# Kernel optimization log

Hardware: AMD Instinct MI355X
Metric: run time of the kernel (lower is better)

The kernel has to match this reference:

```python
import jax, jax.numpy as jnp
import numpy as np

HIDDEN = 1024
HEADS = 16
HEAD_DIM = HIDDEN // HEADS
POS_DIM = 128
B, S = 2, 2048
ROPE_BASE = 10000.0


def setup_inputs() -> dict:
    key = jax.random.key(0)
    ks = jax.random.split(key, 8)
    sd = 1.0 / np.sqrt(HIDDEN)
    return {
        "x":   jax.random.normal(ks[0], (B, S, HIDDEN), dtype=jnp.float32),
        "W_q": jax.random.normal(ks[1], (HIDDEN, HIDDEN), dtype=jnp.float32) * sd,
        "W_k": jax.random.normal(ks[2], (HIDDEN, HIDDEN), dtype=jnp.float32) * sd,
        "W_v": jax.random.normal(ks[3], (HIDDEN, HIDDEN), dtype=jnp.float32) * sd,
        "W_o": jax.random.normal(ks[4], (HIDDEN, HIDDEN), dtype=jnp.float32) * sd,
        "repo_W1": jax.random.normal(ks[5], (HIDDEN, POS_DIM), dtype=jnp.float32) * sd,
        "repo_b1": jnp.zeros((POS_DIM,), dtype=jnp.float32),
        "repo_W2": jax.random.normal(ks[6], (POS_DIM, 1), dtype=jnp.float32) * (1.0 / np.sqrt(POS_DIM)),
        "repo_b2": jnp.zeros((1,), dtype=jnp.float32),
    }


def _repo_positions(x, W1, b1, W2, b2):
    # 2-layer MLP -> scalar per token; softplus + cumsum gives monotone learned positions
    h = jax.nn.gelu(jnp.einsum("bsd,dp->bsp", x, W1) + b1)
    raw = (jnp.einsum("bsp,po->bso", h, W2) + b2)[..., 0]      # (B, S)
    return jnp.cumsum(jax.nn.softplus(raw), axis=1)             # (B, S)


def _apply_rope(q, k, positions):
    # q, k: (B, S, H, Dh); positions: (B, S) continuous
    half = HEAD_DIM // 2
    inv_freq = 1.0 / (ROPE_BASE ** (jnp.arange(0, HEAD_DIM, 2, dtype=jnp.float32) / HEAD_DIM))
    angles = positions[:, :, None] * inv_freq                   # (B, S, half)
    cos = jnp.cos(angles)[:, :, None, :]                        # (B, S, 1, half)
    sin = jnp.sin(angles)[:, :, None, :]

    def rot(t):
        t1, t2 = t[..., :half], t[..., half:]
        return jnp.concatenate([t1 * cos - t2 * sin, t1 * sin + t2 * cos], axis=-1)

    return rot(q), rot(k)


def reference(x, W_q, W_k, W_v, W_o, repo_W1, repo_b1, repo_W2, repo_b2):
    scale = 1.0 / np.sqrt(HEAD_DIM)
    q = jnp.einsum("bsd,de->bse", x, W_q).reshape(B, S, HEADS, HEAD_DIM)
    k = jnp.einsum("bsd,de->bse", x, W_k).reshape(B, S, HEADS, HEAD_DIM)
    v = jnp.einsum("bsd,de->bse", x, W_v).reshape(B, S, HEADS, HEAD_DIM)

    positions = _repo_positions(x, repo_W1, repo_b1, repo_W2, repo_b2)
    q, k = _apply_rope(q, k, positions)

    # explicit O(S^2) attention, matching the torch module
    scores = jnp.einsum("bqhd,bkhd->bhqk", q, k) * scale        # (B, H, S, S)
    attn = jax.nn.softmax(scores, axis=-1)
    out = jnp.einsum("bhqk,bkhd->bqhd", attn, v)                # (B, S, H, Dh)
    out = out.reshape(B, S, HIDDEN)
    return jnp.einsum("bsd,de->bse", out, W_o)
```

## Files before the change

### kernel.cpp

```cpp
#include <hip/hip_runtime.h>
#include <hip/hip_bf16.h>
#include <math.h>

#define HIDDEN 1024
#define HEADS 16
#define HEAD_DIM 64
#define POS_DIM 128
#define BATCH 2
#define SEQ 2048
#define TOKENS (BATCH * SEQ)

typedef _Float16 f16;
typedef __attribute__((ext_vector_type(8))) _Float16 f16x8;
typedef __attribute__((ext_vector_type(4))) _Float16 f16x4;
typedef __attribute__((ext_vector_type(4))) float f32x4;

__device__ __forceinline__ void glds16(const f16* g, f16* l) {
    __builtin_amdgcn_global_load_lds((const __attribute__((address_space(1))) unsigned int*)g,
                                     (__attribute__((address_space(3))) unsigned int*)l, 16, 0, 0);
}

__global__ __launch_bounds__(256) void cast_x_kernel(const float* __restrict__ x,
                                                     f16* __restrict__ o) {
    const int i = (blockIdx.x * 256 + threadIdx.x) * 8;
    const float4 u = *(const float4*)(x + i);
    const float4 v = *(const float4*)(x + i + 4);
    f16x8 r = {(f16)u.x, (f16)u.y, (f16)u.z, (f16)u.w,
               (f16)v.x, (f16)v.y, (f16)v.z, (f16)v.w};
    *(f16x8*)(o + i) = r;
}

__global__ __launch_bounds__(256) void cast_wt4_kernel(const float* __restrict__ W0,
                                                       const float* __restrict__ W1,
                                                       const float* __restrict__ W2,
                                                       const float* __restrict__ W3,
                                                       f16* __restrict__ Wt) {
    __shared__ float ts[32][33];
    const int t = threadIdx.x;
    const int z = blockIdx.z;
    const float* W = (z == 0) ? W0 : (z == 1) ? W1 : (z == 2) ? W2 : W3;
    f16* dst = Wt + (size_t)z * HIDDEN * HIDDEN;
    const int k0 = blockIdx.y * 32, n0 = blockIdx.x * 32;
    {
        const int r = t >> 3, c4 = (t & 7) * 4;
        const float4 u = *(const float4*)(W + (size_t)(k0 + r) * HIDDEN + n0 + c4);
        ts[r][c4 + 0] = u.x; ts[r][c4 + 1] = u.y; ts[r][c4 + 2] = u.z; ts[r][c4 + 3] = u.w;
    }
    __syncthreads();
    {
        const int r = t >> 3, c4 = (t & 7) * 4;
        f16* o = dst + (size_t)(n0 + r) * HIDDEN + k0 + c4;
        o[0] = (f16)ts[c4 + 0][r]; o[1] = (f16)ts[c4 + 1][r];
        o[2] = (f16)ts[c4 + 2][r]; o[3] = (f16)ts[c4 + 3][r];
    }
}

__global__ __launch_bounds__(256) void cast_w1t_kernel(const float* __restrict__ W1,
                                                       f16* __restrict__ Wh,
                                                       f16* __restrict__ Wl) {
    __shared__ float ts[32][33];
    const int t = threadIdx.x;
    const int k0 = blockIdx.y * 32, p0 = blockIdx.x * 32;
    {
        const int r = t >> 3, c4 = (t & 7) * 4;
        const float4 u = *(const float4*)(W1 + (size_t)(k0 + r) * POS_DIM + p0 + c4);
        ts[r][c4 + 0] = u.x; ts[r][c4 + 1] = u.y; ts[r][c4 + 2] = u.z; ts[r][c4 + 3] = u.w;
    }
    __syncthreads();
    {
        const int r = t >> 3, c4 = (t & 7) * 4;
        f16* oh = Wh + (size_t)(p0 + r) * HIDDEN + k0 + c4;
        f16* ol = Wl + (size_t)(p0 + r) * HIDDEN + k0 + c4;
#pragma unroll
        for (int u = 0; u < 4; ++u) {
            const float v = ts[c4 + u][r];
            const f16 hi = (f16)v;
            oh[u] = hi;
            ol[u] = (f16)(v - (float)hi);
        }
    }
}

__global__ __launch_bounds__(256, 3) void gemm_gll(const f16* __restrict__ A,
                                                   const f16* __restrict__ Bt,
                                                   f16* __restrict__ Cb,
                                                   float* __restrict__ Cf,
                                                   int N, int f16out) {
    __shared__ __align__(16) f16 As[128 * 64];
    __shared__ __align__(16) f16 Bs[128 * 64];
    const int tid = threadIdx.x;
    const int w = tid >> 6, lane = tid & 63;
    const int g = lane >> 4, c = lane & 15;
    const int m0 = blockIdx.y * 128, n0 = blockIdx.x * 128;
    const int wm = (w & 1) * 64, wn = (w >> 1) * 64;

    const int lrow = lane >> 3;
    const int lseg = (lane & 7) ^ lrow;
    const f16* gA = A + (size_t)(m0 + w * 32 + lrow) * 1024 + lseg * 8;
    const f16* gB = Bt + (size_t)(n0 + w * 32 + lrow) * 1024 + lseg * 8;
    f16* lA = &As[(w * 32) * 64];
    f16* lB = &Bs[(w * 32) * 64];

    f32x4 acc[4][4];
    const f32x4 z = {0.f, 0.f, 0.f, 0.f};
#pragma unroll
    for (int i = 0; i < 4; ++i)
#pragma unroll
        for (int j = 0; j < 4; ++j) acc[i][j] = z;

    const int rsw = c & 7;
    for (int k0 = 0; k0 < 1024; k0 += 64) {
        __syncthreads();
#pragma unroll
        for (int p = 0; p < 4; ++p) {
            glds16(gA + (size_t)p * 8 * 1024 + k0, lA + p * 8 * 64);
            glds16(gB + (size_t)p * 8 * 1024 + k0, lB + p * 8 * 64);
        }
        __syncthreads();
#pragma unroll
        for (int s = 0; s < 2; ++s) {
            f16x8 af[4], bf[4];
#pragma unroll
            for (int i = 0; i < 4; ++i)
                af[i] = *(const f16x8*)&As[(wm + i * 16 + c) * 64 + (((s * 4 + g) ^ rsw) * 8)];
#pragma unroll
            for (int j = 0; j < 4; ++j)
                bf[j] = *(const f16x8*)&Bs[(wn + j * 16 + c) * 64 + (((s * 4 + g) ^ rsw) * 8)];
#pragma unroll
            for (int i = 0; i < 4; ++i)
#pragma unroll
                for (int j = 0; j < 4; ++j)
                    acc[i][j] = __builtin_amdgcn_mfma_f32_16x16x32_f16(af[i], bf[j], acc[i][j], 0, 0, 0);
        }
    }
#pragma unroll
    for (int i = 0; i < 4; ++i)
#pragma unroll
        for (int j = 0; j < 4; ++j)
#pragma unroll
            for (int r = 0; r < 4; ++r) {
                const size_t off = (size_t)(m0 + wm + i * 16 + 4 * g + r) * N + n0 + wn + j * 16 + c;
                if (f16out) Cb[off] = (f16)acc[i][j][r];
                else Cf[off] = acc[i][j][r];
            }
}

__device__ __forceinline__ float gelu_tanh(float x) {
    const float kA = 0.7978845608028654f;
    return 0.5f * x * (1.0f + tanhf(kA * (x + 0.044715f * x * x * x)));
}

__global__ __launch_bounds__(256, 2) void repo_mfma(const float* __restrict__ x,
                                                    const f16* __restrict__ w1h,
                                                    const f16* __restrict__ w1l,
                                                    const float* __restrict__ b1,
                                                    const float* __restrict__ W2,
                                                    const float* __restrict__ b2,
                                                    float* __restrict__ raw) {
    __shared__ __align__(16) f16 Ash[64 * 32], Asl[64 * 32];
    __shared__ __align__(16) f16 Bsh[128 * 32], Bsl[128 * 32];
    __shared__ float red[4][64];
    const int tid = threadIdx.x;
    const int w = tid >> 6, lane = tid & 63;
    const int g = lane >> 4, c = lane & 15;
    const int m0 = blockIdx.x * 64;

    const int arow = tid >> 2, aseg = tid & 3;
    const int aslot = (aseg ^ ((arow ^ (arow >> 2)) & 3)) << 3;
    const float* gA = x + (size_t)(m0 + arow) * 1024 + aseg * 8;
    const f16* gBh0 = w1h + (size_t)arow * 1024 + aseg * 8;
    const f16* gBh1 = w1h + (size_t)(arow + 64) * 1024 + aseg * 8;
    const f16* gBl0 = w1l + (size_t)arow * 1024 + aseg * 8;
    const f16* gBl1 = w1l + (size_t)(arow + 64) * 1024 + aseg * 8;
    f16* sAh = &Ash[arow * 32 + aslot];
    f16* sAl = &Asl[arow * 32 + aslot];
    f16* sBh0 = &Bsh[arow * 32 + aslot];
    f16* sBh1 = &Bsh[(arow + 64) * 32 + aslot];
    f16* sBl0 = &Bsl[arow * 32 + aslot];
    f16* sBl1 = &Bsl[(arow + 64) * 32 + aslot];

    const int foff = ((g ^ ((c ^ (c >> 2)) & 3)) << 3);

    f32x4 acc[4][2];
    const f32x4 z = {0.f, 0.f, 0.f, 0.f};
#pragma unroll
    for (int i = 0; i < 4; ++i) { acc[i][0] = z; acc[i][1] = z; }

    float4 pa0 = *(const float4*)gA;
    float4 pa1 = *(const float4*)(gA + 4);
    f16x8 pbh0 = *(const f16x8*)gBh0, pbh1 = *(const f16x8*)gBh1;
    f16x8 pbl0 = *(const f16x8*)gBl0, pbl1 = *(const f16x8*)gBl1;

    for (int k0 = 0; k0 < 1024; k0 += 32) {
        __syncthreads();
        {
            const float av[8] = {pa0.x, pa0.y, pa0.z, pa0.w, pa1.x, pa1.y, pa1.z, pa1.w};
            f16x8 ah, al;
#pragma unroll
            for (int u = 0; u < 8; ++u) {
                const f16 hi = (f16)av[u];
                ah[u] = hi;
                al[u] = (f16)(av[u] - (float)hi);
            }
            *(f16x8*)sAh = ah; *(f16x8*)sAl = al;
            *(f16x8*)sBh0 = pbh0; *(f16x8*)sBh1 = pbh1;
            *(f16x8*)sBl0 = pbl0; *(f16x8*)sBl1 = pbl1;
        }
        __syncthreads();
        if (k0 + 32 < 1024) {
            pa0 = *(const float4*)(gA + k0 + 32);
            pa1 = *(const float4*)(gA + k0 + 36);
            pbh0 = *(const f16x8*)(gBh0 + k0 + 32);
            pbh1 = *(const f16x8*)(gBh1 + k0 + 32);
            pbl0 = *(const f16x8*)(gBl0 + k0 + 32);
            pbl1 = *(const f16x8*)(gBl1 + k0 + 32);
        }
        f16x8 ah[4], al[4], bh[2], bl[2];
#pragma unroll
        for (int i = 0; i < 4; ++i) {
            ah[i] = *(const f16x8*)&Ash[(i * 16 + c) * 32 + foff];
            al[i] = *(const f16x8*)&Asl[(i * 16 + c) * 32 + foff];
        }
#pragma unroll
        for (int j = 0; j < 2; ++j) {
            bh[j] = *(const f16x8*)&Bsh[(w * 32 + j * 16 + c) * 32 + foff];
            bl[j] = *(const f16x8*)&Bsl[(w * 32 + j * 16 + c) * 32 + foff];
        }
#pragma unroll
        for (int i = 0; i < 4; ++i)
#pragma unroll
            for (int j = 0; j < 2; ++j) {
                acc[i][j] = __builtin_amdgcn_mfma_f32_16x16x32_f16(ah[i], bh[j], acc[i][j], 0, 0, 0);
                acc[i][j] = __builtin_amdgcn_mfma_f32_16x16x32_f16(ah[i], bl[j], acc[i][j], 0, 0, 0);
                acc[i][j] = __builtin_amdgcn_mfma_f32_16x16x32_f16(al[i], bh[j], acc[i][j], 0, 0, 0);
            }
    }
    float b1v[2], w2v[2];
#pragma unroll
    for (int j = 0; j < 2; ++j) {
        const int col = w * 32 + j * 16 + c;
        b1v[j] = b1[col];
        w2v[j] = W2[col];
    }
    float part[4][4];
#pragma unroll
    for (int i = 0; i < 4; ++i)
#pragma unroll
        for (int r = 0; r < 4; ++r) {
            float s = 0.f;
#pragma unroll
            for (int j = 0; j < 2; ++j)
                s += gelu_tanh(acc[i][j][r] + b1v[j]) * w2v[j];
            s += __shfl_xor(s, 1, 64);
            s += __shfl_xor(s, 2, 64);
            s += __shfl_xor(s, 4, 64);
            s += __shfl_xor(s, 8, 64);
            part[i][r] = s;
        }
    if (c == 0)
#pragma unroll
        for (int i = 0; i < 4; ++i)
#pragma unroll
            for (int r = 0; r < 4; ++r)
                red[w][i * 16 + 4 * g + r] = part[i][r];
    __syncthreads();
    if (tid < 64)
        raw[m0 + tid] = red[0][tid] + red[1][tid] + red[2][tid] + red[3][tid] + b2[0];
}

__device__ __forceinline__ double softplus_d(double x) {
    return (x > 0.0) ? x + log1p(exp(-x)) : log1p(exp(x));
}

__global__ __launch_bounds__(256) void repo_cumsum_kernel(const float* __restrict__ raw,
                                                          float* __restrict__ pos) {
    __shared__ double bufA[256];
    __shared__ double bufB[256];
    const int b = blockIdx.x;
    const int t = threadIdx.x;
    const float* r = raw + (size_t)b * SEQ;

    double loc[8];
    double sum = 0.0;
#pragma unroll
    for (int i = 0; i < 8; ++i) {
        sum += softplus_d((double)r[t * 8 + i]);
        loc[i] = sum;
    }
    bufA[t] = sum;
    __syncthreads();

    double* src = bufA;
    double* dst = bufB;
    for (int off = 1; off < 256; off <<= 1) {
        double v = src[t];
        if (t >= off) v += src[t - off];
        dst[t] = v;
        __syncthreads();
        double* tmp = src; src = dst; dst = tmp;
    }
    const double excl = src[t] - sum;
#pragma unroll
    for (int i = 0; i < 8; ++i)
        pos[(size_t)b * SEQ + t * 8 + i] = (float)(excl + loc[i]);
}

__global__ __launch_bounds__(256) void sctab_kernel(const float* __restrict__ pos,
                                                    float* __restrict__ costab,
                                                    float* __restrict__ sintab) {
    const int idx = blockIdx.x * 256 + threadIdx.x;
    const int tok = idx >> 5, i = idx & 31;
    const double ang = (double)pos[tok] * exp(-(double)i * 0.28782313662425574);
    double sa, ca;
    sincos(ang, &sa, &ca);
    costab[idx] = (float)ca;
    sintab[idx] = (float)sa;
}

__global__ __launch_bounds__(256) void packkv_kernel(f16* __restrict__ qkv,
                                                     const float* __restrict__ costab,
                                                     const float* __restrict__ sintab,
                                                     f16* __restrict__ kfo,
                                                     f16* __restrict__ vfo) {
    __shared__ __align__(16) f16 kds[64][72];
    __shared__ __align__(16) f16 vds[64][72];
    const int t = threadIdx.x;
    const int s0 = blockIdx.x * 64;
    const int h = blockIdx.y, b = blockIdx.z;
    const int key = t >> 2, part = t & 3;
    const int tok = b * SEQ + s0 + key;
    {
        float cs[8], sn[8];
        *(float4*)cs       = *(const float4*)(costab + tok * 32 + part * 8);
        *(float4*)(cs + 4) = *(const float4*)(costab + tok * 32 + part * 8 + 4);
        *(float4*)sn       = *(const float4*)(sintab + tok * 32 + part * 8);
        *(float4*)(sn + 4) = *(const float4*)(sintab + tok * 32 + part * 8 + 4);
        f16* qrow = qkv + (size_t)tok * 3072 + h * HEAD_DIM;
        {
            f16x8 lo = *(const f16x8*)(qrow + part * 8);
            f16x8 hi = *(const f16x8*)(qrow + part * 8 + 32);
#pragma unroll
            for (int u = 0; u < 8; ++u) {
                const float l = (float)lo[u], hh = (float)hi[u];
                lo[u] = (f16)(l * cs[u] - hh * sn[u]);
                hi[u] = (f16)(l * sn[u] + hh * cs[u]);
            }
            *(f16x8*)(qrow + part * 8) = lo;
            *(f16x8*)(qrow + part * 8 + 32) = hi;
        }
        const f16* krow = qrow + 1024;
        {
            f16x8 lo = *(const f16x8*)(krow + part * 8);
            f16x8 hi = *(const f16x8*)(krow + part * 8 + 32);
#pragma unroll
            for (int u = 0; u < 8; ++u) {
                const float l = (float)lo[u], hh = (float)hi[u];
                kds[key][part * 8 + u]      = (f16)(l * cs[u] - hh * sn[u]);
                kds[key][32 + part * 8 + u] = (f16)(l * sn[u] + hh * cs[u]);
            }
        }
        const f16* vrow = qrow + 2048;
        f16x8 v0 = *(const f16x8*)(vrow + part * 16);
        f16x8 v1 = *(const f16x8*)(vrow + part * 16 + 8);
#pragma unroll
        for (int u = 0; u < 8; ++u) {
            vds[part * 16 + u][key] = v0[u];
            vds[part * 16 + 8 + u][key] = v1[u];
        }
    }
    __syncthreads();
    const size_t cb = ((size_t)((b * HEADS + h) * 32) + blockIdx.x) * 4096;
#pragma unroll
    for (int p = 0; p < 2; ++p) {
        const int idx = p * 256 + t;
        const int frag = idx >> 6, lane = idx & 63;
        const int jn = frag >> 1, half = frag & 1, g = lane >> 4, c = lane & 15;
        *(f16x8*)(kfo + cb + frag * 512 + lane * 8) =
            *(const f16x8*)(&kds[jn * 16 + c][half * 32 + g * 8]);
    }
#pragma unroll
    for (int p = 0; p < 4; ++p) {
        const int idx = p * 256 + t;
        const int frag = idx >> 6, lane = idx & 63;
        const int jd = frag >> 2, jn = frag & 3, g = lane >> 4, c = lane & 15;
        *(f16x4*)(vfo + cb + frag * 256 + lane * 4) =
            *(const f16x4*)(&vds[jd * 16 + c][jn * 16 + 4 * g]);
    }
}

__global__ __launch_bounds__(256, 2) void attn_f16(const f16* __restrict__ qkv,
                                                   const f16* __restrict__ kfr,
                                                   const f16* __restrict__ vfr,
                                                   f16* __restrict__ aof0,
                                                   f16* __restrict__ aof1,
                                                   float* __restrict__ lsb) {
    __shared__ __align__(16) f16 kls[4096];
    __shared__ __align__(16) f16 vls[4096];
    __shared__ __align__(16) f16 ot[4][32][72];
    const int tid = threadIdx.x;
    const int w = tid >> 6, lane = tid & 63;
    const int g = lane >> 4, c = lane & 15;

    const int wid = blockIdx.x;
    const int xcd = wid & 7, slot = wid >> 3;
    const int combo = xcd * 8 + (slot >> 4);
    const int xblk = slot & 15;
    const int h = combo & 15;
    const int zz = combo >> 4;
    const int b = zz >> 1, half = zz & 1;

    const int bh = b * HEADS + h;
    const int row0 = xblk * 128 + w * 32;
    const int ch0 = half * 16;

    const f16* qb = qkv + (size_t)(b * SEQ + row0) * 3072 + h * HEAD_DIM + g * 8;
    const f16* kfb = kfr + (size_t)bh * 32 * 4096;
    const f16* vfb = vfr + (size_t)bh * 32 * 4096;

    f16x8 qf[2][2];
#pragma unroll
    for (int i = 0; i < 2; ++i) {
        qf[i][0] = *(const f16x8*)(qb + (size_t)(i * 16 + c) * 3072);
        qf[i][1] = *(const f16x8*)(qb + (size_t)(i * 16 + c) * 3072 + 32);
    }
    const f32x4 z = {0.f, 0.f, 0.f, 0.f};
    f32x4 acc[4][2];
    f32x4 accl[2];
#pragma unroll
    for (int jd = 0; jd < 4; ++jd) { acc[jd][0] = z; acc[jd][1] = z; }
    accl[0] = z; accl[1] = z;

    const f16x4 ones = {(f16)1.f, (f16)1.f, (f16)1.f, (f16)1.f};
    const float SC = 0.125f * 1.4426950408889634f;

    for (int cc = 0; cc < 16; ++cc) {
        const int ch = ch0 + cc;
        __syncthreads();
        {
            const f16* kg = kfb + (size_t)ch * 4096 + w * 1024 + lane * 8;
            const f16* vg = vfb + (size_t)ch * 4096 + w * 1024 + lane * 8;
            glds16(kg, kls + w * 1024);
            glds16(kg + 512, kls + w * 1024 + 512);
            glds16(vg, vls + w * 1024);
            glds16(vg + 512, vls + w * 1024 + 512);
        }
        __syncthreads();

        f16x8 kf[8];
        f16x4 vf[16];
#pragma unroll
        for (int f = 0; f < 8; ++f) kf[f] = *(const f16x8*)(kls + lane * 8 + f * 512);
#pragma unroll
        for (int f = 0; f < 16; ++f) vf[f] = *(const f16x4*)(vls + lane * 4 + f * 256);

#pragma unroll
        for (int i = 0; i < 2; ++i) {
            f32x4 s[4];
#pragma unroll
            for (int jn = 0; jn < 4; ++jn) {
                s[jn] = __builtin_amdgcn_mfma_f32_16x16x32_f16(kf[jn * 2], qf[i][0], z, 0, 0, 0);
                s[jn] = __builtin_amdgcn_mfma_f32_16x16x32_f16(kf[jn * 2 + 1], qf[i][1], s[jn], 0, 0, 0);
            }
#pragma unroll
            for (int jn = 0; jn < 4; ++jn) {
                f16x4 pf;
#pragma unroll
                for (int r = 0; r < 4; ++r)
                    pf[r] = (f16)__builtin_amdgcn_exp2f(fmaf(s[jn][r], SC, -8.0f));
                accl[i] = __builtin_amdgcn_mfma_f32_16x16x16f16(ones, pf, accl[i], 0, 0, 0);
#pragma unroll
                for (int jd = 0; jd < 4; ++jd)
                    acc[jd][i] = __builtin_amdgcn_mfma_f32_16x16x16f16(vf[jd * 4 + jn], pf, acc[jd][i], 0, 0, 0);
            }
        }
    }

    if (lane < 16) {
#pragma unroll
        for (int i = 0; i < 2; ++i)
            lsb[((size_t)(half * 32 + bh)) * SEQ + row0 + i * 16 + lane] = accl[i][0];
    }
#pragma unroll
    for (int i = 0; i < 2; ++i)
#pragma unroll
        for (int jd = 0; jd < 4; ++jd)
#pragma unroll
            for (int r = 0; r < 4; ++r)
                ot[w][i * 16 + c][jd * 16 + 4 * g + r] = (f16)acc[jd][i][r];
    f16* aofH = half ? aof1 : aof0;
    const int tr = lane >> 1, hf = lane & 1;
    f16* aob = aofH + (size_t)(b * SEQ + row0 + tr) * HIDDEN + h * HEAD_DIM + hf * 32;
#pragma unroll
    for (int q = 0; q < 4; ++q)
        *(f16x8*)(aob + q * 8) = *(const f16x8*)(&ot[w][tr][hf * 32 + q * 8]);
}

__global__ __launch_bounds__(256) void combine_kernel(f16* __restrict__ a0,
                                                      const f16* __restrict__ a1,
                                                      const float* __restrict__ lsb) {
    const int idx = blockIdx.x * 256 + threadIdx.x;
    const int part = idx & 127;
    const int tok = idx >> 7;
    const int h = part >> 3, d8 = (part & 7) * 8;
    const int b = tok >> 11, s = tok & 2047;
    const size_t li = (size_t)(b * HEADS + h) * SEQ + s;
    const float inv = 1.0f / (lsb[li] + lsb[32 * SEQ + li]);
    const size_t off = (size_t)tok * HIDDEN + h * HEAD_DIM + d8;
    const f16x8 u = *(const f16x8*)(a0 + off);
    const f16x8 v = *(const f16x8*)(a1 + off);
    f16x8 o;
#pragma unroll
    for (int q = 0; q < 8; ++q) o[q] = (f16)(((float)u[q] + (float)v[q]) * inv);
    *(f16x8*)(a0 + off) = o;
}

extern "C" void kernel_launch(void* const* d_in, const int* in_sizes, int n_in,
                              void* d_out, int out_size, void* d_ws, size_t ws_size,
                              hipStream_t stream) {
    const float* x   = (const float*)d_in[0];
    const float* W_q = (const float*)d_in[1];
    const float* W_k = (const float*)d_in[2];
    const float* W_v = (const float*)d_in[3];
    const float* W_o = (const float*)d_in[4];
    const float* rW1 = (const float*)d_in[5];
    const float* rb1 = (const float*)d_in[6];
    const float* rW2 = (const float*)d_in[7];
    const float* rb2 = (const float*)d_in[8];
    float* out = (float*)d_out;

    const size_t MAT = (size_t)TOKENS * HIDDEN;
    const size_t WSZ = (size_t)HIDDEN * HIDDEN;
    f16* x16  = (f16*)d_ws;
    f16* wqkv = x16 + MAT;
    f16* wot  = wqkv + 3 * WSZ;
    f16* qkv  = wot + WSZ;
    f16* kfr  = qkv + 3 * MAT;
    f16* vfr  = kfr + MAT;
    f16* aof0 = vfr + MAT;
    f16* aof1 = aof0 + MAT;
    f16* w1h  = aof1 + MAT;
    f16* w1l  = w1h + POS_DIM * HIDDEN;
    float* raw    = (float*)(w1l + POS_DIM * HIDDEN);
    float* pos    = raw + TOKENS;
    float* costab = pos + TOKENS;
    float* sintab = costab + TOKENS * 32;
    float* lsb    = sintab + TOKENS * 32;

    cast_x_kernel<<<MAT / 2048, 256, 0, stream>>>(x, x16);
    cast_wt4_kernel<<<dim3(32, 32, 4), 256, 0, stream>>>(W_q, W_k, W_v, W_o, wqkv);
    cast_w1t_kernel<<<dim3(4, 32), 256, 0, stream>>>(rW1, w1h, w1l);

    gemm_gll<<<dim3(24, 32), 256, 0, stream>>>(x16, wqkv, qkv, nullptr, 3072, 1);

    repo_mfma<<<64, 256, 0, stream>>>(x, w1h, w1l, rb1, rW2, rb2, raw);
    repo_cumsum_kernel<<<BATCH, 256, 0, stream>>>(raw, pos);
    sctab_kernel<<<TOKENS * 32 / 256, 256, 0, stream>>>(pos, costab, sintab);

    packkv_kernel<<<dim3(SEQ / 64, HEADS, BATCH), 256, 0, stream>>>(qkv, costab, sintab, kfr, vfr);

    attn_f16<<<dim3(1024), 256, 0, stream>>>(qkv, kfr, vfr, aof0, aof1, lsb);
    combine_kernel<<<TOKENS * 128 / 256, 256, 0, stream>>>(aof0, aof1, lsb);

    gemm_gll<<<dim3(8, 32), 256, 0, stream>>>(aof0, wot, nullptr, out, 1024, 0);
}
```

Baseline: 256.6 us.

## Drop KV split in attention, normalize in-kernel and remove combine pass

Each attention block now walks all 32 key chunks instead of splitting the keys across two blocks. That removes the partial output buffers, the row-sum buffer and the separate combine kernel. The softmax denominator is now accumulated in fp32 registers and reduced across lanes with shuffles, replacing the extra ones-MFMA. The grid halves to 512 blocks, so occupancy and parallelism drop, in exchange for less global traffic, one fewer launch and fewer MFMAs.

```diff
diff --git a/kernel.cpp b/kernel.cpp
--- a/kernel.cpp
+++ b/kernel.cpp
@@ -391,9 +391,7 @@
 __global__ __launch_bounds__(256, 2) void attn_f16(const f16* __restrict__ qkv,
                                                    const f16* __restrict__ kfr,
                                                    const f16* __restrict__ vfr,
-                                                   f16* __restrict__ aof0,
-                                                   f16* __restrict__ aof1,
-                                                   float* __restrict__ lsb) {
+                                                   f16* __restrict__ aof0) {
     __shared__ __align__(16) f16 kls[4096];
     __shared__ __align__(16) f16 vls[4096];
     __shared__ __align__(16) f16 ot[4][32][72];
@@ -403,15 +401,13 @@
 
     const int wid = blockIdx.x;
     const int xcd = wid & 7, slot = wid >> 3;
-    const int combo = xcd * 8 + (slot >> 4);
+    const int combo = xcd * 4 + (slot >> 4);
     const int xblk = slot & 15;
     const int h = combo & 15;
-    const int zz = combo >> 4;
-    const int b = zz >> 1, half = zz & 1;
+    const int b = combo >> 4;
 
     const int bh = b * HEADS + h;
     const int row0 = xblk * 128 + w * 32;
-    const int ch0 = half * 16;
 
     const f16* qb = qkv + (size_t)(b * SEQ + row0) * 3072 + h * HEAD_DIM + g * 8;
     const f16* kfb = kfr + (size_t)bh * 32 * 4096;
@@ -425,20 +421,17 @@
     }
     const f32x4 z = {0.f, 0.f, 0.f, 0.f};
     f32x4 acc[4][2];
-    f32x4 accl[2];
 #pragma unroll
     for (int jd = 0; jd < 4; ++jd) { acc[jd][0] = z; acc[jd][1] = z; }
-    accl[0] = z; accl[1] = z;
-
-    const f16x4 ones = {(f16)1.f, (f16)1.f, (f16)1.f, (f16)1.f};
+    float dloc[2] = {0.f, 0.f};
+
     const float SC = 0.125f * 1.4426950408889634f;
 
-    for (int cc = 0; cc < 16; ++cc) {
-        const int ch = ch0 + cc;
+    for (int cc = 0; cc < 32; ++cc) {
         __syncthreads();
         {
-            const f16* kg = kfb + (size_t)ch * 4096 + w * 1024 + lane * 8;
-            const f16* vg = vfb + (size_t)ch * 4096 + w * 1024 + lane * 8;
+            const f16* kg = kfb + (size_t)cc * 4096 + w * 1024 + lane * 8;
+            const f16* vg = vfb + (size_t)cc * 4096 + w * 1024 + lane * 8;
             glds16(kg, kls + w * 1024);
             glds16(kg + 512, kls + w * 1024 + 512);
             glds16(vg, vls + w * 1024);
@@ -463,11 +456,12 @@
             }
 #pragma unroll
             for (int jn = 0; jn < 4; ++jn) {
-                f16x4 pf;
-#pragma unroll
-                for (int r = 0; r < 4; ++r)
-                    pf[r] = (f16)__builtin_amdgcn_exp2f(fmaf(s[jn][r], SC, -8.0f));
-                accl[i] = __builtin_amdgcn_mfma_f32_16x16x16f16(ones, pf, accl[i], 0, 0, 0);
+                const float e0 = __builtin_amdgcn_exp2f(fmaf(s[jn][0], SC, -8.0f));
+                const float e1 = __builtin_amdgcn_exp2f(fmaf(s[jn][1], SC, -8.0f));
+                const float e2 = __builtin_amdgcn_exp2f(fmaf(s[jn][2], SC, -8.0f));
+                const float e3 = __builtin_amdgcn_exp2f(fmaf(s[jn][3], SC, -8.0f));
+                dloc[i] += (e0 + e1) + (e2 + e3);
+                f16x4 pf = {(f16)e0, (f16)e1, (f16)e2, (f16)e3};
 #pragma unroll
                 for (int jd = 0; jd < 4; ++jd)
                     acc[jd][i] = __builtin_amdgcn_mfma_f32_16x16x16f16(vf[jd * 4 + jn], pf, acc[jd][i], 0, 0, 0);
@@ -475,43 +469,26 @@
         }
     }
 
-    if (lane < 16) {
-#pragma unroll
-        for (int i = 0; i < 2; ++i)
-            lsb[((size_t)(half * 32 + bh)) * SEQ + row0 + i * 16 + lane] = accl[i][0];
-    }
+    float inv[2];
+#pragma unroll
+    for (int i = 0; i < 2; ++i) {
+        dloc[i] += __shfl_xor(dloc[i], 16, 64);
+        dloc[i] += __shfl_xor(dloc[i], 32, 64);
+        inv[i] = 1.0f / dloc[i];
+    }
+
 #pragma unroll
     for (int i = 0; i < 2; ++i)
 #pragma unroll
         for (int jd = 0; jd < 4; ++jd)
 #pragma unroll
             for (int r = 0; r < 4; ++r)
-                ot[w][i * 16 + c][jd * 16 + 4 * g + r] = (f16)acc[jd][i][r];
-    f16* aofH = half ? aof1 : aof0;
+                ot[w][i * 16 + c][jd * 16 + 4 * g + r] = (f16)(acc[jd][i][r] * inv[i]);
     const int tr = lane >> 1, hf = lane & 1;
-    f16* aob = aofH + (size_t)(b * SEQ + row0 + tr) * HIDDEN + h * HEAD_DIM + hf * 32;
+    f16* aob = aof0 + (size_t)(b * SEQ + row0 + tr) * HIDDEN + h * HEAD_DIM + hf * 32;
 #pragma unroll
     for (int q = 0; q < 4; ++q)
         *(f16x8*)(aob + q * 8) = *(const f16x8*)(&ot[w][tr][hf * 32 + q * 8]);
-}
-
-__global__ __launch_bounds__(256) void combine_kernel(f16* __restrict__ a0,
-                                                      const f16* __restrict__ a1,
-                                                      const float* __restrict__ lsb) {
-    const int idx = blockIdx.x * 256 + threadIdx.x;
-    const int part = idx & 127;
-    const int tok = idx >> 7;
-    const int h = part >> 3, d8 = (part & 7) * 8;
-    const int b = tok >> 11, s = tok & 2047;
-    const size_t li = (size_t)(b * HEADS + h) * SEQ + s;
-    const float inv = 1.0f / (lsb[li] + lsb[32 * SEQ + li]);
-    const size_t off = (size_t)tok * HIDDEN + h * HEAD_DIM + d8;
-    const f16x8 u = *(const f16x8*)(a0 + off);
-    const f16x8 v = *(const f16x8*)(a1 + off);
-    f16x8 o;
-#pragma unroll
-    for (int q = 0; q < 8; ++q) o[q] = (f16)(((float)u[q] + (float)v[q]) * inv);
-    *(f16x8*)(a0 + off) = o;
 }
 
 extern "C" void kernel_launch(void* const* d_in, const int* in_sizes, int n_in,
@@ -544,7 +521,6 @@
     float* pos    = raw + TOKENS;
     float* costab = pos + TOKENS;
     float* sintab = costab + TOKENS * 32;
-    float* lsb    = sintab + TOKENS * 32;
 
     cast_x_kernel<<<MAT / 2048, 256, 0, stream>>>(x, x16);
     cast_wt4_kernel<<<dim3(32, 32, 4), 256, 0, stream>>>(W_q, W_k, W_v, W_o, wqkv);
@@ -558,8 +534,7 @@
 
     packkv_kernel<<<dim3(SEQ / 64, HEADS, BATCH), 256, 0, stream>>>(qkv, costab, sintab, kfr, vfr);
 
-    attn_f16<<<dim3(1024), 256, 0, stream>>>(qkv, kfr, vfr, aof0, aof1, lsb);
-    combine_kernel<<<TOKENS * 128 / 256, 256, 0, stream>>>(aof0, aof1, lsb);
+    attn_f16<<<dim3(512), 256, 0, stream>>>(qkv, kfr, vfr, aof0);
 
     gemm_gll<<<dim3(8, 32), 256, 0, stream>>>(aof0, wot, nullptr, out, 1024, 0);
 }
```

Measured after the change: 251.6 us. No clear change (-1.9%).
